# Kernel tuning notes

Measured on AMD Instinct MI355X. Metric: run time of the kernel, lower is better.

The kernel has to match this reference:

```python
import jax, jax.numpy as jnp
import numpy as np

N_NODES = 100000
N_EDGES = 3200000
IN_DIM = 512
OUT_DIM = 128


def setup_inputs() -> dict:
    key = jax.random.key(0)
    kx, kw, kr, kc, kv = jax.random.split(key, 5)
    x = jax.random.normal(kx, (N_NODES, IN_DIM), dtype=jnp.float32)
    # glorot uniform init for the weight, matching glorot_init in the source
    init_range = np.sqrt(6.0 / (IN_DIM + OUT_DIM)).astype(np.float32)
    W = jax.random.uniform(kw, (IN_DIM, OUT_DIM), dtype=jnp.float32,
                           minval=-init_range, maxval=init_range)
    edge_row = jax.random.randint(kr, (N_EDGES,), 0, N_NODES, dtype=jnp.int32)
    edge_col = jax.random.randint(kc, (N_EDGES,), 0, N_NODES, dtype=jnp.int32)
    edge_val = jax.random.uniform(kv, (N_EDGES,), dtype=jnp.float32)
    return {"x": x, "W": W, "edge_row": edge_row, "edge_col": edge_col,
            "edge_val": edge_val}


def reference(x, W, edge_row, edge_col, edge_val):
    # dense projection: [N, in] @ [in, out] -> [N, out]
    xp = x @ W
    # SpMM: out[r] += val * xp[c] for each edge (r, c, val)
    msgs = xp[edge_col] * edge_val[:, None]          # [E, out]
    agg = jax.ops.segment_sum(msgs, edge_row, num_segments=N_NODES)
    return jax.nn.relu(agg)
```

## Files before the change

kernel.cpp:

```cpp
#include <hip/hip_runtime.h>

#define M_NODES 100000
#define MPAD    100096
#define K_DIM   512
#define N_DIM   128
#define NUM_EDGES 3200000

#define RSHIFT  6
#define ROWS_PB 64
#define NBUCK   1563
#define BCAP    2432
#define EPW     4096
#define NAPPEND ((NUM_EDGES + EPW - 1) / EPW)
#define GEMM_BLOCKS (MPAD / 128)

#define BK      32
#define KSTEPS  (K_DIM / BK)
#define ABYTES  16384
#define WBYTES  8192
#define BUFBYTES (ABYTES + WBYTES)

typedef __bf16 bf16x8 __attribute__((ext_vector_type(8)));
typedef float f32x16 __attribute__((ext_vector_type(16)));
typedef unsigned short ushort8 __attribute__((ext_vector_type(8)));
typedef unsigned int uint32;

typedef __attribute__((address_space(1))) const unsigned int gas_u32;
typedef __attribute__((address_space(3))) unsigned int las_u32;

__device__ __forceinline__ unsigned short f2bf(float f) {
  uint32 u = __float_as_uint(f);
  u = (u + 0x7FFFu + ((u >> 16) & 1u)) >> 16;
  return (unsigned short)u;
}

__device__ __forceinline__ float bf_lo(uint32 m) {
  return __uint_as_float(m << 16);
}
__device__ __forceinline__ float bf_hi(uint32 m) {
  return __uint_as_float(m & 0xFFFF0000u);
}

__global__ __launch_bounds__(256) void wfrag_kernel(
    const float* __restrict__ W, unsigned short* __restrict__ Wf,
    int* __restrict__ gcursor) {
  const int t = blockIdx.x * 256 + threadIdx.x;
  const int j = t & 7;
  const int lane = (t >> 3) & 63;
  const int ng = (t >> 9) & 3;
  const int ks = t >> 11;
  const int k = ks * 16 + ((lane >> 5) << 3) + j;
  const int n = (ng << 5) + (lane & 31);
  Wf[t] = f2bf(W[k * N_DIM + n]);
  if (t < NBUCK) gcursor[t] = 0;
}

__device__ __forceinline__ void stage_a(float* dst,
                                        const float* __restrict__ x,
                                        int row0, int k0, int w, int lane) {
#pragma unroll
  for (int i = 0; i < 4; ++i) {
    const int seg = i * 4 + w;
    const int d = seg * 1024 + lane * 16;
    const int row = d >> 7;
    const int ch = (d >> 4) & 7;
    const int sch = ch ^ (row & 7);
    int gr = row0 + row;
    if (gr >= M_NODES) gr = M_NODES - 1;
    const float* src = x + (size_t)gr * K_DIM + k0 + sch * 4;
    __builtin_amdgcn_global_load_lds((gas_u32*)src,
                                     (las_u32*)(dst + seg * 256), 16, 0, 0);
  }
}

__device__ __forceinline__ void stage_w(unsigned short* dst,
                                        const unsigned short* __restrict__ Wf,
                                        int t, int w, int lane) {
#pragma unroll
  for (int i = 0; i < 2; ++i) {
    const int seg = i * 4 + w;
    const unsigned short* src =
        Wf + (size_t)t * 4096 + seg * 512 + lane * 8;
    __builtin_amdgcn_global_load_lds((gas_u32*)src,
                                     (las_u32*)(dst + seg * 512), 16, 0, 0);
  }
}

__device__ __forceinline__ bf16x8 read_a_frag(const float* As, int r, int ks,
                                              int hi) {
  const int c0 = ks * 4 + hi * 2;
  const int sw = r & 7;
  const float4 f0 = *(const float4*)(As + r * 32 + ((c0 ^ sw) << 2));
  const float4 f1 = *(const float4*)(As + r * 32 + (((c0 + 1) ^ sw) << 2));
  ushort8 u;
  u[0] = f2bf(f0.x); u[1] = f2bf(f0.y); u[2] = f2bf(f0.z); u[3] = f2bf(f0.w);
  u[4] = f2bf(f1.x); u[5] = f2bf(f1.y); u[6] = f2bf(f1.z); u[7] = f2bf(f1.w);
  return __builtin_bit_cast(bf16x8, u);
}

__device__ __forceinline__ void gemm_body(int bx, char* smem,
                                          const float* __restrict__ x,
                                          const unsigned short* __restrict__ Wf,
                                          unsigned short* __restrict__ xp) {
  float* A0 = (float*)smem;
  unsigned short* W0 = (unsigned short*)(smem + ABYTES);
  float* A1 = (float*)(smem + BUFBYTES);
  unsigned short* W1 = (unsigned short*)(smem + BUFBYTES + ABYTES);

  const int tid = threadIdx.x;
  const int w = tid >> 6;
  const int lane = tid & 63;
  const int l31 = lane & 31;
  const int lhi = lane >> 5;
  const int row0 = bx * 128;
  const int r = w * 32 + l31;

  f32x16 acc[4] = {};

  stage_a(A0, x, row0, 0, w, lane);
  stage_w(W0, Wf, 0, w, lane);

  for (int t = 0; t < KSTEPS; ++t) {
    float* Ac = (t & 1) ? A1 : A0;
    unsigned short* Wc = (t & 1) ? W1 : W0;
    if (t + 1 < KSTEPS) {
      float* An = (t & 1) ? A0 : A1;
      unsigned short* Wn = (t & 1) ? W0 : W1;
      stage_a(An, x, row0, (t + 1) * BK, w, lane);
      stage_w(Wn, Wf, t + 1, w, lane);
      asm volatile("s_waitcnt vmcnt(6)" ::: "memory");
    } else {
      asm volatile("s_waitcnt vmcnt(0)" ::: "memory");
    }
    __builtin_amdgcn_s_barrier();

#pragma unroll
    for (int ks = 0; ks < 2; ++ks) {
      const bf16x8 a = read_a_frag(Ac, r, ks, lhi);
      const ushort8* bp = (const ushort8*)Wc + (size_t)ks * 4 * 64 + lane;
#pragma unroll
      for (int ng = 0; ng < 4; ++ng) {
        const bf16x8 b = __builtin_bit_cast(bf16x8, bp[(size_t)ng * 64]);
        acc[ng] =
            __builtin_amdgcn_mfma_f32_32x32x16_bf16(a, b, acc[ng], 0, 0, 0);
      }
    }
    __builtin_amdgcn_s_barrier();
  }

  const int rbase = row0 + w * 32 + 4 * lhi;
#pragma unroll
  for (int ng = 0; ng < 4; ++ng) {
    const int cc = (ng << 5) + l31;
#pragma unroll
    for (int reg = 0; reg < 16; ++reg) {
      const int rr = rbase + (reg & 3) + 8 * (reg >> 2);
      xp[(size_t)rr * N_DIM + cc] = f2bf(acc[ng][reg]);
    }
  }
}

__device__ __forceinline__ int tag_edge(int r, int* lcnt) {
  const int b = r >> RSHIFT;
  const int s = atomicAdd(&lcnt[b], 1);
  return (b << 18) | (s << 6) | (r & (ROWS_PB - 1));
}

__device__ __forceinline__ void emit_edge(int p, int col, float v,
                                          const int* lbase,
                                          uint2* __restrict__ buckets) {
  const int b = (int)((unsigned)p >> 18);
  const int idx = lbase[b] + ((p >> 6) & 0xFFF);
  if (idx < BCAP)
    buckets[(size_t)b * BCAP + idx] = make_uint2(
        ((uint32)col << 6) | (uint32)(p & (ROWS_PB - 1)), __float_as_uint(v));
}

__device__ __forceinline__ void bin_body(int bx, char* smem,
                                         const int* __restrict__ erow,
                                         const int* __restrict__ ecol,
                                         const float* __restrict__ eval,
                                         int* __restrict__ gcursor,
                                         uint2* __restrict__ buckets) {
  int* lcnt = (int*)smem;
  int* lbase = (int*)(smem + 6912);
  const int tid = threadIdx.x;
  for (int i = tid; i < NBUCK; i += 256) lcnt[i] = 0;
  __syncthreads();

  const int base = bx * EPW;
  int pk[16];
#pragma unroll
  for (int c = 0; c < 4; ++c) {
    const int e0 = base + c * 1024 + tid * 4;
    if (e0 < NUM_EDGES) {
      const int4 r4 = *(const int4*)(erow + e0);
      pk[c * 4 + 0] = tag_edge(r4.x, lcnt);
      pk[c * 4 + 1] = tag_edge(r4.y, lcnt);
      pk[c * 4 + 2] = tag_edge(r4.z, lcnt);
      pk[c * 4 + 3] = tag_edge(r4.w, lcnt);
    }
  }
  __syncthreads();

  for (int i = tid; i < NBUCK; i += 256) {
    const int c = lcnt[i];
    lbase[i] = c ? atomicAdd(&gcursor[i], c) : 0;
  }
  __syncthreads();

#pragma unroll
  for (int c = 0; c < 4; ++c) {
    const int e0 = base + c * 1024 + tid * 4;
    if (e0 < NUM_EDGES) {
      const int4 c4 = *(const int4*)(ecol + e0);
      const float4 v4 = *(const float4*)(eval + e0);
      emit_edge(pk[c * 4 + 0], c4.x, v4.x, lbase, buckets);
      emit_edge(pk[c * 4 + 1], c4.y, v4.y, lbase, buckets);
      emit_edge(pk[c * 4 + 2], c4.z, v4.z, lbase, buckets);
      emit_edge(pk[c * 4 + 3], c4.w, v4.w, lbase, buckets);
    }
  }
}

__global__ __launch_bounds__(256) void gemm_bin_kernel(
    const float* __restrict__ x, const unsigned short* __restrict__ Wf,
    unsigned short* __restrict__ xp, const int* __restrict__ erow,
    const int* __restrict__ ecol, const float* __restrict__ eval,
    int* __restrict__ gcursor, uint2* __restrict__ buckets) {
  __shared__ __align__(16) char smem[2 * BUFBYTES];
  if (blockIdx.x < GEMM_BLOCKS) {
    gemm_body(blockIdx.x, smem, x, Wf, xp);
  } else {
    bin_body(blockIdx.x - GEMM_BLOCKS, smem, erow, ecol, eval, gcursor,
             buckets);
  }
}

__global__ __launch_bounds__(256, 8) void bucket_gather_kernel(
    const unsigned short* __restrict__ xp, const int* __restrict__ gcursor,
    const uint2* __restrict__ buckets, float* __restrict__ out) {
  __shared__ uint2 eds[BCAP];
  __shared__ int rbase[ROWS_PB + 1];
  __shared__ int rcur[ROWS_PB];
  __shared__ int stmp[ROWS_PB];

  const int b = blockIdx.x;
  const int tid = threadIdx.x;
  int n = gcursor[b];
  if (n > BCAP) n = BCAP;

  if (tid < ROWS_PB) rcur[tid] = 0;
  __syncthreads();

  const uint2* bk = buckets + (size_t)b * BCAP;
  for (int i = tid; i < n; i += 256) atomicAdd(&rcur[bk[i].x & 63], 1);
  __syncthreads();

  if (tid < ROWS_PB) stmp[tid] = rcur[tid];
  __syncthreads();
  for (int off = 1; off < ROWS_PB; off <<= 1) {
    int v = 0, a = 0;
    if (tid < ROWS_PB) {
      v = stmp[tid];
      if (tid >= off) a = stmp[tid - off];
    }
    __syncthreads();
    if (tid < ROWS_PB) stmp[tid] = v + a;
    __syncthreads();
  }
  if (tid < ROWS_PB) {
    rbase[tid + 1] = stmp[tid];
    rcur[tid] = 0;
  }
  if (tid == 0) rbase[0] = 0;
  __syncthreads();

  for (int i = tid; i < n; i += 256) {
    const uint2 e = bk[i];
    const int rl = e.x & 63;
    const int pos = rbase[rl] + atomicAdd(&rcur[rl], 1);
    eds[pos] = e;
  }
  __syncthreads();

  const int wv = tid >> 6;
  const int lane = tid & 63;
  const uint32* xpl = (const uint32*)xp + lane;

  for (int rl = wv; rl < ROWS_PB; rl += 4) {
    const int row = (b << RSHIFT) + rl;
    if (row >= M_NODES) break;
    const int s = rbase[rl];
    const int e = rbase[rl + 1];

    float ax0 = 0.f, ay0 = 0.f, ax1 = 0.f, ay1 = 0.f;
    float ax2 = 0.f, ay2 = 0.f, ax3 = 0.f, ay3 = 0.f;
    int i = s;
    for (; i + 3 < e; i += 4) {
      const uint2 e0 = eds[i];
      const uint2 e1 = eds[i + 1];
      const uint2 e2 = eds[i + 2];
      const uint2 e3 = eds[i + 3];
      const uint32 m0 = xpl[(size_t)(e0.x >> 6) * 64];
      const uint32 m1 = xpl[(size_t)(e1.x >> 6) * 64];
      const uint32 m2 = xpl[(size_t)(e2.x >> 6) * 64];
      const uint32 m3 = xpl[(size_t)(e3.x >> 6) * 64];
      const float v0 = __uint_as_float(e0.y);
      const float v1 = __uint_as_float(e1.y);
      const float v2 = __uint_as_float(e2.y);
      const float v3 = __uint_as_float(e3.y);
      ax0 += v0 * bf_lo(m0); ay0 += v0 * bf_hi(m0);
      ax1 += v1 * bf_lo(m1); ay1 += v1 * bf_hi(m1);
      ax2 += v2 * bf_lo(m2); ay2 += v2 * bf_hi(m2);
      ax3 += v3 * bf_lo(m3); ay3 += v3 * bf_hi(m3);
    }
    for (; i < e; ++i) {
      const uint2 e0 = eds[i];
      const uint32 m0 = xpl[(size_t)(e0.x >> 6) * 64];
      const float v0 = __uint_as_float(e0.y);
      ax0 += v0 * bf_lo(m0);
      ay0 += v0 * bf_hi(m0);
    }

    float2 r;
    r.x = fmaxf((ax0 + ax1) + (ax2 + ax3), 0.f);
    r.y = fmaxf((ay0 + ay1) + (ay2 + ay3), 0.f);
    *(float2*)(out + (size_t)row * N_DIM + lane * 2) = r;
  }
}

extern "C" void kernel_launch(void* const* d_in, const int* in_sizes, int n_in,
                              void* d_out, int out_size, void* d_ws,
                              size_t ws_size, hipStream_t stream) {
  const float* x = (const float*)d_in[0];
  const float* W = (const float*)d_in[1];
  const int* erow = (const int*)d_in[2];
  const int* ecol = (const int*)d_in[3];
  const float* eval = (const float*)d_in[4];
  float* out = (float*)d_out;

  char* wsb = (char*)d_ws;
  size_t off = 0;
  auto alloc = [&](size_t bytes) {
    char* p = wsb + off;
    off = (off + bytes + 511) & ~(size_t)511;
    return p;
  };
  unsigned short* xp =
      (unsigned short*)alloc((size_t)MPAD * N_DIM * sizeof(unsigned short));
  unsigned short* Wf =
      (unsigned short*)alloc((size_t)K_DIM * N_DIM * sizeof(unsigned short));
  int* gcursor = (int*)alloc((size_t)NBUCK * sizeof(int));
  uint2* buckets = (uint2*)alloc((size_t)NBUCK * BCAP * sizeof(uint2));
  (void)ws_size;

  wfrag_kernel<<<(K_DIM * N_DIM) / 256, 256, 0, stream>>>(W, Wf, gcursor);

  gemm_bin_kernel<<<GEMM_BLOCKS + NAPPEND, 256, 0, stream>>>(
      x, Wf, xp, erow, ecol, eval, gcursor, buckets);

  bucket_gather_kernel<<<NBUCK, 256, 0, stream>>>(xp, gcursor, buckets, out);
}
```

Measured before the change: 474.1 us.

## Enlarge binning blocks, pad global bucket cursors, and schedule bin blocks first

Each binning block now processes four times as many edges, so far fewer atomics hit the global bucket cursors. Those cursors are padded to one per 64-byte line to avoid contention between neighbouring buckets. Per-edge slot tags are no longer kept in registers; instead the row array is re-read and slots are reassigned with a second pass of shared atomics. Binning blocks are now dispatched before the GEMM blocks in the fused launch, which changes how the two kinds of work overlap.

```diff
diff --git a/kernel.cpp b/kernel.cpp
--- a/kernel.cpp
+++ b/kernel.cpp
@@ -10,9 +10,10 @@
 #define ROWS_PB 64
 #define NBUCK   1563
 #define BCAP    2432
-#define EPW     4096
+#define EPW     16384
 #define NAPPEND ((NUM_EDGES + EPW - 1) / EPW)
 #define GEMM_BLOCKS (MPAD / 128)
+#define GCUR_STRIDE 16
 
 #define BK      32
 #define KSTEPS  (K_DIM / BK)
@@ -52,7 +53,7 @@
   const int k = ks * 16 + ((lane >> 5) << 3) + j;
   const int n = (ng << 5) + (lane & 31);
   Wf[t] = f2bf(W[k * N_DIM + n]);
-  if (t < NBUCK) gcursor[t] = 0;
+  if (t < NBUCK * GCUR_STRIDE) gcursor[t] = 0;
 }
 
 __device__ __forceinline__ void stage_a(float* dst,
@@ -160,20 +161,15 @@
   }
 }
 
-__device__ __forceinline__ int tag_edge(int r, int* lcnt) {
+__device__ __forceinline__ void place_edge(int r, int col, float v,
+                                           const int* lbase, int* lcur,
+                                           uint2* __restrict__ buckets) {
   const int b = r >> RSHIFT;
-  const int s = atomicAdd(&lcnt[b], 1);
-  return (b << 18) | (s << 6) | (r & (ROWS_PB - 1));
-}
-
-__device__ __forceinline__ void emit_edge(int p, int col, float v,
-                                          const int* lbase,
-                                          uint2* __restrict__ buckets) {
-  const int b = (int)((unsigned)p >> 18);
-  const int idx = lbase[b] + ((p >> 6) & 0xFFF);
+  const int s = atomicAdd(&lcur[b], 1);
+  const int idx = lbase[b] + s;
   if (idx < BCAP)
     buckets[(size_t)b * BCAP + idx] = make_uint2(
-        ((uint32)col << 6) | (uint32)(p & (ROWS_PB - 1)), __float_as_uint(v));
+        ((uint32)col << 6) | (uint32)(r & (ROWS_PB - 1)), __float_as_uint(v));
 }
 
 __device__ __forceinline__ void bin_body(int bx, char* smem,
@@ -189,36 +185,37 @@
   __syncthreads();
 
   const int base = bx * EPW;
-  int pk[16];
-#pragma unroll
-  for (int c = 0; c < 4; ++c) {
+
+  for (int c = 0; c < 16; ++c) {
     const int e0 = base + c * 1024 + tid * 4;
     if (e0 < NUM_EDGES) {
       const int4 r4 = *(const int4*)(erow + e0);
-      pk[c * 4 + 0] = tag_edge(r4.x, lcnt);
-      pk[c * 4 + 1] = tag_edge(r4.y, lcnt);
-      pk[c * 4 + 2] = tag_edge(r4.z, lcnt);
-      pk[c * 4 + 3] = tag_edge(r4.w, lcnt);
+      atomicAdd(&lcnt[r4.x >> RSHIFT], 1);
+      atomicAdd(&lcnt[r4.y >> RSHIFT], 1);
+      atomicAdd(&lcnt[r4.z >> RSHIFT], 1);
+      atomicAdd(&lcnt[r4.w >> RSHIFT], 1);
     }
   }
   __syncthreads();
 
   for (int i = tid; i < NBUCK; i += 256) {
     const int c = lcnt[i];
-    lbase[i] = c ? atomicAdd(&gcursor[i], c) : 0;
-  }
-  __syncthreads();
-
-#pragma unroll
-  for (int c = 0; c < 4; ++c) {
+    lbase[i] = c ? atomicAdd(&gcursor[i * GCUR_STRIDE], c) : 0;
+  }
+  __syncthreads();
+  for (int i = tid; i < NBUCK; i += 256) lcnt[i] = 0;
+  __syncthreads();
+
+  for (int c = 0; c < 16; ++c) {
     const int e0 = base + c * 1024 + tid * 4;
     if (e0 < NUM_EDGES) {
+      const int4 r4 = *(const int4*)(erow + e0);
       const int4 c4 = *(const int4*)(ecol + e0);
       const float4 v4 = *(const float4*)(eval + e0);
-      emit_edge(pk[c * 4 + 0], c4.x, v4.x, lbase, buckets);
-      emit_edge(pk[c * 4 + 1], c4.y, v4.y, lbase, buckets);
-      emit_edge(pk[c * 4 + 2], c4.z, v4.z, lbase, buckets);
-      emit_edge(pk[c * 4 + 3], c4.w, v4.w, lbase, buckets);
+      place_edge(r4.x, c4.x, v4.x, lbase, lcnt, buckets);
+      place_edge(r4.y, c4.y, v4.y, lbase, lcnt, buckets);
+      place_edge(r4.z, c4.z, v4.z, lbase, lcnt, buckets);
+      place_edge(r4.w, c4.w, v4.w, lbase, lcnt, buckets);
     }
   }
 }
@@ -229,11 +226,10 @@
     const int* __restrict__ ecol, const float* __restrict__ eval,
     int* __restrict__ gcursor, uint2* __restrict__ buckets) {
   __shared__ __align__(16) char smem[2 * BUFBYTES];
-  if (blockIdx.x < GEMM_BLOCKS) {
-    gemm_body(blockIdx.x, smem, x, Wf, xp);
+  if (blockIdx.x < NAPPEND) {
+    bin_body(blockIdx.x, smem, erow, ecol, eval, gcursor, buckets);
   } else {
-    bin_body(blockIdx.x - GEMM_BLOCKS, smem, erow, ecol, eval, gcursor,
-             buckets);
+    gemm_body(blockIdx.x - NAPPEND, smem, x, Wf, xp);
   }
 }
 
@@ -247,7 +243,7 @@
 
   const int b = blockIdx.x;
   const int tid = threadIdx.x;
-  int n = gcursor[b];
+  int n = gcursor[b * GCUR_STRIDE];
   if (n > BCAP) n = BCAP;
 
   if (tid < ROWS_PB) rcur[tid] = 0;
@@ -351,7 +347,7 @@
       (unsigned short*)alloc((size_t)MPAD * N_DIM * sizeof(unsigned short));
   unsigned short* Wf =
       (unsigned short*)alloc((size_t)K_DIM * N_DIM * sizeof(unsigned short));
-  int* gcursor = (int*)alloc((size_t)NBUCK * sizeof(int));
+  int* gcursor = (int*)alloc((size_t)NBUCK * GCUR_STRIDE * sizeof(int));
   uint2* buckets = (uint2*)alloc((size_t)NBUCK * BCAP * sizeof(uint2));
   (void)ws_size;
 
```

Result: slower. 491.4 us (+3.7%).

## Stage binned edges in LDS sorted by bucket and pad global cursors

Applied to the files above, without the earlier changes.

The binning blocks now do a block-wide prefix scan over per-bucket counts and place each edge record into a bucket-sorted LDS staging area. A second pass writes the records out contiguously, using a binary search over the scanned offsets to find each record's bucket. This replaces scattered 8-byte global stores with writes that group into per-bucket runs. Global bucket cursors are also padded to 64-byte stride to avoid atomic contention on shared cache lines. In exchange it adds an LDS scan, extra barriers and a per-record binary search (about 11 steps).

```diff
diff --git a/kernel.cpp b/kernel.cpp
--- a/kernel.cpp
+++ b/kernel.cpp
@@ -13,12 +13,19 @@
 #define EPW     4096
 #define NAPPEND ((NUM_EDGES + EPW - 1) / EPW)
 #define GEMM_BLOCKS (MPAD / 128)
+#define GCUR_STRIDE 16
 
 #define BK      32
 #define KSTEPS  (K_DIM / BK)
 #define ABYTES  16384
 #define WBYTES  8192
 #define BUFBYTES (ABYTES + WBYTES)
+#define SMEM_BYTES (2 * BUFBYTES)
+
+#define BIN_LBASE_OFF 6912
+#define BIN_REC_OFF   13824
+#define BIN_WPART_OFF 46592
+#define SCAN_CHUNK    7
 
 typedef __bf16 bf16x8 __attribute__((ext_vector_type(8)));
 typedef float f32x16 __attribute__((ext_vector_type(16)));
@@ -52,7 +59,7 @@
   const int k = ks * 16 + ((lane >> 5) << 3) + j;
   const int n = (ng << 5) + (lane & 31);
   Wf[t] = f2bf(W[k * N_DIM + n]);
-  if (t < NBUCK) gcursor[t] = 0;
+  if (t < NBUCK * GCUR_STRIDE) gcursor[t] = 0;
 }
 
 __device__ __forceinline__ void stage_a(float* dst,
@@ -166,16 +173,6 @@
   return (b << 18) | (s << 6) | (r & (ROWS_PB - 1));
 }
 
-__device__ __forceinline__ void emit_edge(int p, int col, float v,
-                                          const int* lbase,
-                                          uint2* __restrict__ buckets) {
-  const int b = (int)((unsigned)p >> 18);
-  const int idx = lbase[b] + ((p >> 6) & 0xFFF);
-  if (idx < BCAP)
-    buckets[(size_t)b * BCAP + idx] = make_uint2(
-        ((uint32)col << 6) | (uint32)(p & (ROWS_PB - 1)), __float_as_uint(v));
-}
-
 __device__ __forceinline__ void bin_body(int bx, char* smem,
                                          const int* __restrict__ erow,
                                          const int* __restrict__ ecol,
@@ -183,7 +180,10 @@
                                          int* __restrict__ gcursor,
                                          uint2* __restrict__ buckets) {
   int* lcnt = (int*)smem;
-  int* lbase = (int*)(smem + 6912);
+  int* lbase = (int*)(smem + BIN_LBASE_OFF);
+  uint2* rec = (uint2*)(smem + BIN_REC_OFF);
+  int* wpart = (int*)(smem + BIN_WPART_OFF);
+
   const int tid = threadIdx.x;
   for (int i = tid; i < NBUCK; i += 256) lcnt[i] = 0;
   __syncthreads();
@@ -205,7 +205,41 @@
 
   for (int i = tid; i < NBUCK; i += 256) {
     const int c = lcnt[i];
-    lbase[i] = c ? atomicAdd(&gcursor[i], c) : 0;
+    lbase[i] = c ? atomicAdd(&gcursor[i * GCUR_STRIDE], c) : 0;
+  }
+  {
+    int s = 0;
+    const int c0 = tid * SCAN_CHUNK;
+#pragma unroll
+    for (int j = 0; j < SCAN_CHUNK; ++j) {
+      const int i = c0 + j;
+      if (i < NBUCK) s += lcnt[i];
+    }
+    wpart[tid] = s;
+  }
+  __syncthreads();
+
+  for (int off = 1; off < 256; off <<= 1) {
+    const int v = wpart[tid];
+    const int a = (tid >= off) ? wpart[tid - off] : 0;
+    __syncthreads();
+    wpart[tid] = v + a;
+    __syncthreads();
+  }
+  const int n = wpart[255];
+
+  {
+    int run = (tid == 0) ? 0 : wpart[tid - 1];
+    const int c0 = tid * SCAN_CHUNK;
+#pragma unroll
+    for (int j = 0; j < SCAN_CHUNK; ++j) {
+      const int i = c0 + j;
+      if (i < NBUCK) {
+        const int v = lcnt[i];
+        lcnt[i] = run;
+        run += v;
+      }
+    }
   }
   __syncthreads();
 
@@ -215,11 +249,32 @@
     if (e0 < NUM_EDGES) {
       const int4 c4 = *(const int4*)(ecol + e0);
       const float4 v4 = *(const float4*)(eval + e0);
-      emit_edge(pk[c * 4 + 0], c4.x, v4.x, lbase, buckets);
-      emit_edge(pk[c * 4 + 1], c4.y, v4.y, lbase, buckets);
-      emit_edge(pk[c * 4 + 2], c4.z, v4.z, lbase, buckets);
-      emit_edge(pk[c * 4 + 3], c4.w, v4.w, lbase, buckets);
-    }
+#pragma unroll
+      for (int q = 0; q < 4; ++q) {
+        const int p = pk[c * 4 + q];
+        const int b = (int)((unsigned)p >> 18);
+        const int s = (p >> 6) & 0xFFF;
+        const int col = (q == 0) ? c4.x : (q == 1) ? c4.y : (q == 2) ? c4.z
+                                                                     : c4.w;
+        const float v = (q == 0) ? v4.x : (q == 1) ? v4.y : (q == 2) ? v4.z
+                                                                     : v4.w;
+        rec[lcnt[b] + s] = make_uint2(
+            ((uint32)col << 6) | (uint32)(p & (ROWS_PB - 1)),
+            __float_as_uint(v));
+      }
+    }
+  }
+  __syncthreads();
+
+  for (int p = tid; p < n; p += 256) {
+    int lo = 0, hi = NBUCK;
+    while (hi - lo > 1) {
+      const int mid = (lo + hi) >> 1;
+      if (lcnt[mid] <= p) lo = mid; else hi = mid;
+    }
+    const int b = lo;
+    const int idx = lbase[b] + (p - lcnt[b]);
+    if (idx < BCAP) buckets[(size_t)b * BCAP + idx] = rec[p];
   }
 }
 
@@ -228,7 +283,7 @@
     unsigned short* __restrict__ xp, const int* __restrict__ erow,
     const int* __restrict__ ecol, const float* __restrict__ eval,
     int* __restrict__ gcursor, uint2* __restrict__ buckets) {
-  __shared__ __align__(16) char smem[2 * BUFBYTES];
+  __shared__ __align__(16) char smem[SMEM_BYTES];
   if (blockIdx.x < GEMM_BLOCKS) {
     gemm_body(blockIdx.x, smem, x, Wf, xp);
   } else {
@@ -247,7 +302,7 @@
 
   const int b = blockIdx.x;
   const int tid = threadIdx.x;
-  int n = gcursor[b];
+  int n = gcursor[b * GCUR_STRIDE];
   if (n > BCAP) n = BCAP;
 
   if (tid < ROWS_PB) rcur[tid] = 0;
@@ -351,7 +406,7 @@
       (unsigned short*)alloc((size_t)MPAD * N_DIM * sizeof(unsigned short));
   unsigned short* Wf =
       (unsigned short*)alloc((size_t)K_DIM * N_DIM * sizeof(unsigned short));
-  int* gcursor = (int*)alloc((size_t)NBUCK * sizeof(int));
+  int* gcursor = (int*)alloc((size_t)NBUCK * GCUR_STRIDE * sizeof(int));
   uint2* buckets = (uint2*)alloc((size_t)NBUCK * BCAP * sizeof(uint2));
   (void)ws_size;
 
```

Result: slower. 495.4 us (+4.5%).

## Load W fragments into registers, pad bucket cursors, and cap GEMM occupancy

Applied to the files above, without the earlier changes.

The GEMM now reads its pre-swizzled bf16 W fragments straight from global memory into registers each K-step, instead of staging them through LDS. This shrinks shared memory to two A buffers and adjusts the vmcnt wait to match. The bucket cursors are spread to one per 64-byte line to reduce contention among atomics that share a cache line, and the fused kernel gets a launch bound of 4 blocks per CU. The trade-off is extra vector registers and repeated global/L2 reads of W by every block, in exchange for higher possible occupancy and less LDS traffic.

```diff
diff --git a/kernel.cpp b/kernel.cpp
--- a/kernel.cpp
+++ b/kernel.cpp
@@ -13,12 +13,12 @@
 #define EPW     4096
 #define NAPPEND ((NUM_EDGES + EPW - 1) / EPW)
 #define GEMM_BLOCKS (MPAD / 128)
+#define GCUR_STRIDE 16
 
 #define BK      32
 #define KSTEPS  (K_DIM / BK)
 #define ABYTES  16384
-#define WBYTES  8192
-#define BUFBYTES (ABYTES + WBYTES)
+#define SMEM_BYTES (2 * ABYTES)
 
 typedef __bf16 bf16x8 __attribute__((ext_vector_type(8)));
 typedef float f32x16 __attribute__((ext_vector_type(16)));
@@ -52,7 +52,7 @@
   const int k = ks * 16 + ((lane >> 5) << 3) + j;
   const int n = (ng << 5) + (lane & 31);
   Wf[t] = f2bf(W[k * N_DIM + n]);
-  if (t < NBUCK) gcursor[t] = 0;
+  if (t < NBUCK * GCUR_STRIDE) gcursor[t] = 0;
 }
 
 __device__ __forceinline__ void stage_a(float* dst,
@@ -73,19 +73,6 @@
   }
 }
 
-__device__ __forceinline__ void stage_w(unsigned short* dst,
-                                        const unsigned short* __restrict__ Wf,
-                                        int t, int w, int lane) {
-#pragma unroll
-  for (int i = 0; i < 2; ++i) {
-    const int seg = i * 4 + w;
-    const unsigned short* src =
-        Wf + (size_t)t * 4096 + seg * 512 + lane * 8;
-    __builtin_amdgcn_global_load_lds((gas_u32*)src,
-                                     (las_u32*)(dst + seg * 512), 16, 0, 0);
-  }
-}
-
 __device__ __forceinline__ bf16x8 read_a_frag(const float* As, int r, int ks,
                                               int hi) {
   const int c0 = ks * 4 + hi * 2;
@@ -103,9 +90,7 @@
                                           const unsigned short* __restrict__ Wf,
                                           unsigned short* __restrict__ xp) {
   float* A0 = (float*)smem;
-  unsigned short* W0 = (unsigned short*)(smem + ABYTES);
-  float* A1 = (float*)(smem + BUFBYTES);
-  unsigned short* W1 = (unsigned short*)(smem + BUFBYTES + ABYTES);
+  float* A1 = (float*)(smem + ABYTES);
 
   const int tid = threadIdx.x;
   const int w = tid >> 6;
@@ -118,17 +103,26 @@
   f32x16 acc[4] = {};
 
   stage_a(A0, x, row0, 0, w, lane);
-  stage_w(W0, Wf, 0, w, lane);
 
   for (int t = 0; t < KSTEPS; ++t) {
     float* Ac = (t & 1) ? A1 : A0;
-    unsigned short* Wc = (t & 1) ? W1 : W0;
+
+    ushort8 breg[8];
+    const int ksg0 = t * 2;
+#pragma unroll
+    for (int ks = 0; ks < 2; ++ks) {
+#pragma unroll
+      for (int ng = 0; ng < 4; ++ng) {
+        breg[ks * 4 + ng] =
+            ((const ushort8*)Wf)[((size_t)(ksg0 + ks) * 4 + ng) * 64 + lane];
+      }
+    }
+    asm volatile("" ::: "memory");
+
     if (t + 1 < KSTEPS) {
       float* An = (t & 1) ? A0 : A1;
-      unsigned short* Wn = (t & 1) ? W0 : W1;
       stage_a(An, x, row0, (t + 1) * BK, w, lane);
-      stage_w(Wn, Wf, t + 1, w, lane);
-      asm volatile("s_waitcnt vmcnt(6)" ::: "memory");
+      asm volatile("s_waitcnt vmcnt(4)" ::: "memory");
     } else {
       asm volatile("s_waitcnt vmcnt(0)" ::: "memory");
     }
@@ -137,10 +131,9 @@
 #pragma unroll
     for (int ks = 0; ks < 2; ++ks) {
       const bf16x8 a = read_a_frag(Ac, r, ks, lhi);
-      const ushort8* bp = (const ushort8*)Wc + (size_t)ks * 4 * 64 + lane;
 #pragma unroll
       for (int ng = 0; ng < 4; ++ng) {
-        const bf16x8 b = __builtin_bit_cast(bf16x8, bp[(size_t)ng * 64]);
+        const bf16x8 b = __builtin_bit_cast(bf16x8, breg[ks * 4 + ng]);
         acc[ng] =
             __builtin_amdgcn_mfma_f32_32x32x16_bf16(a, b, acc[ng], 0, 0, 0);
       }
@@ -205,7 +198,7 @@
 
   for (int i = tid; i < NBUCK; i += 256) {
     const int c = lcnt[i];
-    lbase[i] = c ? atomicAdd(&gcursor[i], c) : 0;
+    lbase[i] = c ? atomicAdd(&gcursor[i * GCUR_STRIDE], c) : 0;
   }
   __syncthreads();
 
@@ -223,12 +216,12 @@
   }
 }
 
-__global__ __launch_bounds__(256) void gemm_bin_kernel(
+__global__ __launch_bounds__(256, 4) void gemm_bin_kernel(
     const float* __restrict__ x, const unsigned short* __restrict__ Wf,
     unsigned short* __restrict__ xp, const int* __restrict__ erow,
     const int* __restrict__ ecol, const float* __restrict__ eval,
     int* __restrict__ gcursor, uint2* __restrict__ buckets) {
-  __shared__ __align__(16) char smem[2 * BUFBYTES];
+  __shared__ __align__(16) char smem[SMEM_BYTES];
   if (blockIdx.x < GEMM_BLOCKS) {
     gemm_body(blockIdx.x, smem, x, Wf, xp);
   } else {
@@ -247,7 +240,7 @@
 
   const int b = blockIdx.x;
   const int tid = threadIdx.x;
-  int n = gcursor[b];
+  int n = gcursor[b * GCUR_STRIDE];
   if (n > BCAP) n = BCAP;
 
   if (tid < ROWS_PB) rcur[tid] = 0;
@@ -351,7 +344,7 @@
       (unsigned short*)alloc((size_t)MPAD * N_DIM * sizeof(unsigned short));
   unsigned short* Wf =
       (unsigned short*)alloc((size_t)K_DIM * N_DIM * sizeof(unsigned short));
-  int* gcursor = (int*)alloc((size_t)NBUCK * sizeof(int));
+  int* gcursor = (int*)alloc((size_t)NBUCK * GCUR_STRIDE * sizeof(int));
   uint2* buckets = (uint2*)alloc((size_t)NBUCK * BCAP * sizeof(uint2));
   (void)ws_size;
 
```

Measured after the change: 507.1 us. +7.0%, slower.
